# Kernel tuning notes

Measured on AMD Instinct MI355X. Metric: run time of the kernel, lower is better.

Reference implementation:

```python
import jax, jax.numpy as jnp
from jax import lax
import numpy as np

L, D, HEADS, DH, FF = 12, 768, 12, 64, 3072
PATCH, IMG, B, S, OUT = 16, 224, 32, 197, 512


def setup_inputs() -> dict:
    key = jax.random.key(0)
    ks = jax.random.split(key, 10)
    nrm = lambda k, shp, s=0.02: jax.random.normal(k, shp, jnp.float32) * s
    return {
        "x_inp": jax.random.normal(ks[0], (B, 3, IMG, IMG), jnp.float32),
        "conv_w": nrm(ks[1], (D, 3, PATCH, PATCH)),
        "cls_emb": nrm(ks[2], (D,)),
        "pos_emb": nrm(ks[3], (S, D)),
        "ln_pre_w": jnp.ones((D,), jnp.float32),
        "ln_pre_b": jnp.zeros((D,), jnp.float32),
        "ln1_w": jnp.ones((L, D), jnp.float32),
        "ln1_b": jnp.zeros((L, D), jnp.float32),
        "qkv_w": nrm(ks[4], (L, 3 * D, D)),
        "qkv_b": jnp.zeros((L, 3 * D), jnp.float32),
        "out_w": nrm(ks[5], (L, D, D)),
        "out_b": jnp.zeros((L, D), jnp.float32),
        "ln2_w": jnp.ones((L, D), jnp.float32),
        "ln2_b": jnp.zeros((L, D), jnp.float32),
        "fc1_w": nrm(ks[6], (L, FF, D)),
        "fc1_b": jnp.zeros((L, FF), jnp.float32),
        "fc2_w": nrm(ks[7], (L, D, FF)),
        "fc2_b": jnp.zeros((L, D), jnp.float32),
        "ln_post_w": jnp.ones((D,), jnp.float32),
        "ln_post_b": jnp.zeros((D,), jnp.float32),
        "proj": nrm(ks[8], (D, OUT)),
    }


def _ln(x, w, b, eps=1e-5):
    mu = jnp.mean(x, axis=-1, keepdims=True)
    var = jnp.mean(jnp.square(x - mu), axis=-1, keepdims=True)
    return (x - mu) * lax.rsqrt(var + eps) * w + b


def _visual_forward(x_inp, conv_w, cls_emb, pos_emb, ln_pre_w, ln_pre_b,
                    ln1_w, ln1_b, qkv_w, qkv_b, out_w, out_b,
                    ln2_w, ln2_b, fc1_w, fc1_b, fc2_w, fc2_b,
                    ln_post_w, ln_post_b, proj):
    # patch embedding: conv stride=patch, no bias  -> [B, D, 14, 14]
    x = lax.conv_general_dilated(x_inp, conv_w, (PATCH, PATCH), 'VALID',
                                 dimension_numbers=('NCHW', 'OIHW', 'NCHW'))
    b = x.shape[0]
    x = x.reshape(b, D, -1).transpose(0, 2, 1)              # [B, 196, D]
    cls = jnp.broadcast_to(cls_emb, (b, 1, D))
    x = jnp.concatenate([cls, x], axis=1)                   # [B, 197, D]
    x = x + pos_emb[None]                                   # standard 197-token branch
    x = _ln(x, ln_pre_w, ln_pre_b)

    scale = float(DH) ** -0.5

    def block(h, p):
        l1w, l1b, qw, qb, ow, ob, l2w, l2b, f1w, f1b, f2w, f2b = p
        y = _ln(h, l1w, l1b)
        qkv = y @ qw.T + qb                                  # [B, S, 3D]
        q, k, v = jnp.split(qkv, 3, axis=-1)
        q = q.reshape(b, S, HEADS, DH) * scale
        k = k.reshape(b, S, HEADS, DH)
        v = v.reshape(b, S, HEADS, DH)
        attn = jnp.einsum('bqhd,bkhd->bhqk', q, k)
        attn = jax.nn.softmax(attn, axis=-1)
        o = jnp.einsum('bhqk,bkhd->bqhd', attn, v).reshape(b, S, D)
        h = h + o @ ow.T + ob
        y = _ln(h, l2w, l2b)
        y = y @ f1w.T + f1b
        y = y * jax.nn.sigmoid(1.702 * y)                    # QuickGELU
        h = h + y @ f2w.T + f2b
        return h, None

    params = (ln1_w, ln1_b, qkv_w, qkv_b, out_w, out_b,
              ln2_w, ln2_b, fc1_w, fc1_b, fc2_w, fc2_b)
    x, _ = lax.scan(block, x, params)

    cls_out = _ln(x[:, 0, :], ln_post_w, ln_post_b)
    return cls_out @ proj                                    # [B, 512]


def reference(x_inp, conv_w, cls_emb, pos_emb, ln_pre_w, ln_pre_b,
              ln1_w, ln1_b, qkv_w, qkv_b, out_w, out_b,
              ln2_w, ln2_b, fc1_w, fc1_b, fc2_w, fc2_b,
              ln_post_w, ln_post_b, proj):
    return _visual_forward(x_inp, conv_w, cls_emb, pos_emb, ln_pre_w, ln_pre_b,
                           ln1_w, ln1_b, qkv_w, qkv_b, out_w, out_b,
                           ln2_w, ln2_b, fc1_w, fc1_b, fc2_w, fc2_b,
                           ln_post_w, ln_post_b, proj)
```

## Files before the change

kernel.cpp:

```cpp
#include <hip/hip_runtime.h>
#include <hip/hip_bf16.h>


#define LAYERS 12
#define DMODEL 768
#define NHEADS 12
#define DHEAD  64
#define FFDIM  3072
#define BATCH  32
#define SEQ    197
#define NPATCH 196
#define OUTD   512
#define MROWS  (BATCH * SEQ)
#define MPAD   6400
#define SPAD   208
#define VSTR   208

typedef __attribute__((ext_vector_type(4))) float f32x4;
typedef __attribute__((ext_vector_type(8))) short bf16x8;

enum { M_F32 = 0, M_ACC = 1, M_GELU = 2, M_PATCH = 3, M_QKVB = 4 };

__device__ __forceinline__ float b2f(short s) {
    unsigned u = ((unsigned)(unsigned short)s) << 16;
    return __builtin_bit_cast(float, u);
}
__device__ __forceinline__ short f2b(float f) {
    __hip_bfloat16 h = __float2bfloat16(f);
    return __builtin_bit_cast(short, h);
}

__device__ __forceinline__ void gl2lds16(const void* g, void* l) {
    __builtin_amdgcn_global_load_lds(
        (const __attribute__((address_space(1))) void*)g,
        (__attribute__((address_space(3))) void*)l, 16, 0, 0);
}

__global__ __launch_bounds__(256) void cvt_bf16_kernel(
    const float* __restrict__ src, __hip_bfloat16* __restrict__ dst, long n)
{
    long i0 = ((long)blockIdx.x * 256 + threadIdx.x) * 4;
    long stride = (long)gridDim.x * 1024;
    for (long i = i0; i < n; i += stride) {
        float4 v = *reinterpret_cast<const float4*>(&src[i]);
        dst[i + 0] = __float2bfloat16(v.x);
        dst[i + 1] = __float2bfloat16(v.y);
        dst[i + 2] = __float2bfloat16(v.z);
        dst[i + 3] = __float2bfloat16(v.w);
    }
}

__global__ __launch_bounds__(256) void im2col_kernel(
    const float* __restrict__ x_inp, __hip_bfloat16* __restrict__ patches)
{
    int bp = blockIdx.x;
    int b = bp / NPATCH, p = bp % NPATCH;
    int py = p / 14, px = p % 14;
    const float* xb = x_inp + (long)b * 3 * 224 * 224;
    for (int e = threadIdx.x; e < 768; e += 256) {
        int c = e >> 8, i = (e >> 4) & 15, j = e & 15;
        patches[(long)bp * 768 + e] =
            __float2bfloat16(xb[((long)c * 224 + py * 16 + i) * 224 + px * 16 + j]);
    }
}

__global__ __launch_bounds__(256) void cls_token_kernel(
    const float* __restrict__ cls_emb, const float* __restrict__ pos_emb,
    float* __restrict__ x)
{
    int b = blockIdx.x;
    for (int d = threadIdx.x; d < DMODEL; d += 256)
        x[(long)b * SEQ * DMODEL + d] = cls_emb[d] + pos_emb[d];
}

template<int OB>
__global__ __launch_bounds__(256) void ln_kernel(
    const float* __restrict__ in, void* __restrict__ out,
    const float* __restrict__ w, const float* __restrict__ bb,
    long in_stride, long out_stride)
{
    int row = blockIdx.x;
    const float* xr = in + (long)row * in_stride;
    int t = threadIdx.x;
    int lane = t & 63, wid = t >> 6;
    __shared__ float red[8];

    float v[3];
    float s = 0.f;
    #pragma unroll
    for (int i = 0; i < 3; ++i) { v[i] = xr[t + i * 256]; s += v[i]; }
    #pragma unroll
    for (int off = 32; off; off >>= 1) s += __shfl_xor(s, off);
    if (lane == 0) red[wid] = s;
    __syncthreads();
    float mean = (red[0] + red[1] + red[2] + red[3]) * (1.0f / DMODEL);
    float sq = 0.f;
    #pragma unroll
    for (int i = 0; i < 3; ++i) { float d = v[i] - mean; sq += d * d; }
    #pragma unroll
    for (int off = 32; off; off >>= 1) sq += __shfl_xor(sq, off);
    if (lane == 0) red[4 + wid] = sq;
    __syncthreads();
    float rstd = rsqrtf((red[4] + red[5] + red[6] + red[7]) * (1.0f / DMODEL) + 1e-5f);
    #pragma unroll
    for (int i = 0; i < 3; ++i) {
        int d = t + i * 256;
        float o = (v[i] - mean) * rstd * w[d] + bb[d];
        if (OB) ((__hip_bfloat16*)out)[(long)row * out_stride + d] = __float2bfloat16(o);
        else    ((float*)out)[(long)row * out_stride + d] = o;
    }
}

template<int MODE>
__global__ __launch_bounds__(256) void gemm_bf16(
    const __hip_bfloat16* __restrict__ A, const __hip_bfloat16* __restrict__ W,
    const float* __restrict__ bias, float* __restrict__ Cf,
    __hip_bfloat16* __restrict__ Cb, int M, int N, int K, int NB,
    const float* __restrict__ pos)
{
    __shared__ short As[2][64 * 64];
    __shared__ short Bs[2][128 * 64];
    int tid = threadIdx.x, lane = tid & 63, wv = tid >> 6;

    int nwg = gridDim.x, bid = blockIdx.x;
    int qq = nwg >> 3, rr = nwg & 7;
    int xcd = bid & 7, idx = bid >> 3;
    int newid = (xcd < rr ? xcd * (qq + 1) : rr * (qq + 1) + (xcd - rr) * qq) + idx;

    int bm = (newid / NB) * 64, bn = (newid % NB) * 128;
    int wn = wv * 32;
    f32x4 acc[4][2] = {};

    int sr = tid >> 3, sc = tid & 7;
    int c_log = sc ^ (sr & 7);
    const short* Ag = (const short*)A + (long)(bm + sr) * K + (c_log << 3);
    const short* Bg = (const short*)W + (long)(bn + sr) * K + (c_log << 3);
    const long K32 = (long)32 * K;

    int lg = lane >> 4, lr16 = lane & 15;
    int aoff[2][4], boff[2][2];
    #pragma unroll
    for (int s = 0; s < 2; ++s) {
        #pragma unroll
        for (int i = 0; i < 4; ++i) {
            int ra = i * 16 + lr16;
            aoff[s][i] = (ra << 6) + ((((s << 2) | lg) ^ (ra & 7)) << 3);
        }
        #pragma unroll
        for (int j = 0; j < 2; ++j) {
            int rb = wn + j * 16 + lr16;
            boff[s][j] = (rb << 6) + ((((s << 2) | lg) ^ (rb & 7)) << 3);
        }
    }

    const int KT = K >> 6;
    {
        char* Ad = (char*)&As[0][0]; char* Bd = (char*)&Bs[0][0];
        gl2lds16(Ag,           Ad + tid * 16);
        gl2lds16(Ag + K32,     Ad + 4096 + tid * 16);
        gl2lds16(Bg,           Bd + tid * 16);
        gl2lds16(Bg + K32,     Bd + 4096 + tid * 16);
        gl2lds16(Bg + 2 * K32, Bd + 8192 + tid * 16);
        gl2lds16(Bg + 3 * K32, Bd + 12288 + tid * 16);
    }
    __syncthreads();

    int cur = 0;
    for (int t = 0; t < KT; ++t) {
        if (t + 1 < KT) {
            int ktn = (t + 1) << 6;
            char* Ad = (char*)&As[cur ^ 1][0];
            char* Bd = (char*)&Bs[cur ^ 1][0];
            gl2lds16(Ag + ktn,           Ad + tid * 16);
            gl2lds16(Ag + K32 + ktn,     Ad + 4096 + tid * 16);
            gl2lds16(Bg + ktn,           Bd + tid * 16);
            gl2lds16(Bg + K32 + ktn,     Bd + 4096 + tid * 16);
            gl2lds16(Bg + 2 * K32 + ktn, Bd + 8192 + tid * 16);
            gl2lds16(Bg + 3 * K32 + ktn, Bd + 12288 + tid * 16);
        }
        const short* Ab = &As[cur][0];
        const short* Bb = &Bs[cur][0];
        #pragma unroll
        for (int s = 0; s < 2; ++s) {
            bf16x8 af[4], bfr[2];
            #pragma unroll
            for (int i = 0; i < 4; ++i)
                af[i] = *reinterpret_cast<const bf16x8*>(&Ab[aoff[s][i]]);
            #pragma unroll
            for (int j = 0; j < 2; ++j)
                bfr[j] = *reinterpret_cast<const bf16x8*>(&Bb[boff[s][j]]);
            #pragma unroll
            for (int mi = 0; mi < 4; ++mi)
                #pragma unroll
                for (int ni = 0; ni < 2; ++ni)
                    acc[mi][ni] = __builtin_amdgcn_mfma_f32_16x16x32_bf16(
                        af[mi], bfr[ni], acc[mi][ni], 0, 0, 0);
        }
        __syncthreads();
        cur ^= 1;
    }

    #pragma unroll
    for (int mi = 0; mi < 4; ++mi) {
        int row0 = bm + mi * 16 + (lane >> 4) * 4;
        #pragma unroll
        for (int ni = 0; ni < 2; ++ni) {
            int col = bn + wn + ni * 16 + lr16;
            #pragma unroll
            for (int r = 0; r < 4; ++r) {
                int row = row0 + r;
                if (row >= M) continue;
                float v = acc[mi][ni][r];
                if (MODE == M_PATCH) {
                    int pb = row / 196, pp = row - pb * 196;
                    Cf[((long)(pb * SEQ + 1 + pp)) * DMODEL + col] =
                        v + pos[(long)(1 + pp) * DMODEL + col];
                } else {
                    v += bias[col];
                    long idx2 = (long)row * N + col;
                    if (MODE == M_F32)      Cf[idx2] = v;
                    else if (MODE == M_ACC) Cf[idx2] += v;
                    else if (MODE == M_QKVB) Cb[idx2] = __float2bfloat16(v);
                    else if (MODE == M_GELU)
                        Cb[idx2] = __float2bfloat16(v / (1.f + __expf(-1.702f * v)));
                }
            }
        }
    }
}

__global__ __launch_bounds__(256) void attn_kernel(
    const __hip_bfloat16* __restrict__ qkv,
    __hip_bfloat16* __restrict__ o)
{
    int bh = blockIdx.x;
    int b = bh / NHEADS, h = bh % NHEADS;
    int tid = threadIdx.x, lane = tid & 63, wv = tid >> 6;
    __shared__ short Ks[SPAD * 64];
    __shared__ short Vt[64 * VSTR];
    __shared__ short Ps[4][16 * VSTR];
    const short* base = (const short*)qkv + (long)b * SEQ * 2304;

    for (int idx = tid; idx < SPAD * 8; idx += 256) {
        int r = idx >> 3, c = idx & 7;
        int4 val = make_int4(0, 0, 0, 0);
        if (r < SEQ)
            val = *reinterpret_cast<const int4*>(base + (long)r * 2304 + 768 + h * 64 + c * 8);
        *reinterpret_cast<int4*>(&Ks[r * 64 + ((c ^ (r & 7)) << 3)]) = val;
    }
    for (int idx = tid; idx < SPAD * 64; idx += 256) {
        int k = idx >> 6, d = idx & 63;
        short v = (k < SEQ) ? base[(long)k * 2304 + 1536 + h * 64 + d] : (short)0;
        Vt[d * VSTR + k] = v;
    }
    __syncthreads();

    int lg = lane >> 4, lr = lane & 15;
    short* Pw = Ps[wv];

    for (int ch = wv; ch < 13; ch += 4) {
        int q0 = ch * 16;
        const short* qp = (const short*)qkv +
            ((long)(b * SEQ) + q0 + lr) * 2304 + h * 64 + (lg << 3);
        bf16x8 qa = *reinterpret_cast<const bf16x8*>(qp);
        bf16x8 qb = *reinterpret_cast<const bf16x8*>(qp + 32);

        f32x4 sc[13];
        #pragma unroll
        for (int f = 0; f < 13; ++f) sc[f] = (f32x4){0.f, 0.f, 0.f, 0.f};
        #pragma unroll
        for (int f = 0; f < 13; ++f) {
            int row = f * 16 + lr;
            int sw = row & 7;
            const short* kr = &Ks[row * 64];
            bf16x8 k0 = *reinterpret_cast<const bf16x8*>(&kr[((lg + 0) ^ sw) << 3]);
            bf16x8 k1 = *reinterpret_cast<const bf16x8*>(&kr[((lg + 4) ^ sw) << 3]);
            sc[f] = __builtin_amdgcn_mfma_f32_16x16x32_bf16(qa, k0, sc[f], 0, 0, 0);
            sc[f] = __builtin_amdgcn_mfma_f32_16x16x32_bf16(qb, k1, sc[f], 0, 0, 0);
        }

        float mrow[4] = {-1e30f, -1e30f, -1e30f, -1e30f};
        #pragma unroll
        for (int f = 0; f < 13; ++f) {
            bool ok = f * 16 + lr < SEQ;
            #pragma unroll
            for (int r = 0; r < 4; ++r)
                if (ok) mrow[r] = fmaxf(mrow[r], sc[f][r] * 0.125f);
        }
        #pragma unroll
        for (int r = 0; r < 4; ++r)
            #pragma unroll
            for (int off = 8; off; off >>= 1)
                mrow[r] = fmaxf(mrow[r], __shfl_xor(mrow[r], off));
        float esum[4] = {0.f, 0.f, 0.f, 0.f};
        #pragma unroll
        for (int f = 0; f < 13; ++f) {
            bool ok = f * 16 + lr < SEQ;
            #pragma unroll
            for (int r = 0; r < 4; ++r) {
                float e = ok ? __expf(sc[f][r] * 0.125f - mrow[r]) : 0.f;
                sc[f][r] = e;
                esum[r] += e;
            }
        }
        #pragma unroll
        for (int r = 0; r < 4; ++r)
            #pragma unroll
            for (int off = 8; off; off >>= 1)
                esum[r] += __shfl_xor(esum[r], off);
        float inv[4];
        #pragma unroll
        for (int r = 0; r < 4; ++r) inv[r] = 1.0f / esum[r];

        #pragma unroll
        for (int f = 0; f < 13; ++f)
            #pragma unroll
            for (int r = 0; r < 4; ++r)
                Pw[(lg * 4 + r) * VSTR + f * 16 + lr] = f2b(sc[f][r] * inv[r]);

        f32x4 oa[4] = {};
        #pragma unroll
        for (int ks = 0; ks < 7; ++ks) {
            int kb = ks * 32 + (lg << 3);
            bf16x8 pa = {};
            if (kb < SPAD) pa = *reinterpret_cast<const bf16x8*>(&Pw[lr * VSTR + kb]);
            #pragma unroll
            for (int d = 0; d < 4; ++d) {
                bf16x8 vb = {};
                if (kb < SPAD)
                    vb = *reinterpret_cast<const bf16x8*>(&Vt[(d * 16 + lr) * VSTR + kb]);
                oa[d] = __builtin_amdgcn_mfma_f32_16x16x32_bf16(pa, vb, oa[d], 0, 0, 0);
            }
        }

        #pragma unroll
        for (int d = 0; d < 4; ++d)
            #pragma unroll
            for (int r = 0; r < 4; ++r) {
                int q = q0 + lg * 4 + r;
                if (q < SEQ)
                    o[((long)(b * SEQ + q)) * DMODEL + h * 64 + d * 16 + lr] =
                        __float2bfloat16(oa[d][r]);
            }
    }
}

__global__ __launch_bounds__(256) void proj_kernel(
    const float* __restrict__ cls_ln,
    const float* __restrict__ proj,
    float* __restrict__ out)
{
    int idx = blockIdx.x * 256 + threadIdx.x;
    int m = idx >> 9, n = idx & 511;
    float s = 0.f;
    #pragma unroll 8
    for (int k = 0; k < 768; ++k)
        s += cls_ln[m * 768 + k] * proj[k * 512 + n];
    out[idx] = s;
}

extern "C" void kernel_launch(void* const* d_in, const int* in_sizes, int n_in,
                              void* d_out, int out_size, void* d_ws, size_t ws_size,
                              hipStream_t stream) {
    const float* x_inp    = (const float*)d_in[0];
    const float* conv_w   = (const float*)d_in[1];
    const float* cls_emb  = (const float*)d_in[2];
    const float* pos_emb  = (const float*)d_in[3];
    const float* ln_pre_w = (const float*)d_in[4];
    const float* ln_pre_b = (const float*)d_in[5];
    const float* ln1_w    = (const float*)d_in[6];
    const float* ln1_b    = (const float*)d_in[7];
    const float* qkv_w    = (const float*)d_in[8];
    const float* qkv_b    = (const float*)d_in[9];
    const float* out_w    = (const float*)d_in[10];
    const float* out_b    = (const float*)d_in[11];
    const float* ln2_w    = (const float*)d_in[12];
    const float* ln2_b    = (const float*)d_in[13];
    const float* fc1_w    = (const float*)d_in[14];
    const float* fc1_b    = (const float*)d_in[15];
    const float* fc2_w    = (const float*)d_in[16];
    const float* fc2_b    = (const float*)d_in[17];
    const float* ln_post_w= (const float*)d_in[18];
    const float* ln_post_b= (const float*)d_in[19];
    const float* proj     = (const float*)d_in[20];

    char* w = (char*)d_ws;
    __hip_bfloat16* wqkv = (__hip_bfloat16*)w; w += (size_t)LAYERS * 2304 * DMODEL * 2;
    __hip_bfloat16* wout = (__hip_bfloat16*)w; w += (size_t)LAYERS * DMODEL * DMODEL * 2;
    __hip_bfloat16* wfc1 = (__hip_bfloat16*)w; w += (size_t)LAYERS * FFDIM * DMODEL * 2;
    __hip_bfloat16* wfc2 = (__hip_bfloat16*)w; w += (size_t)LAYERS * DMODEL * FFDIM * 2;
    __hip_bfloat16* wconv= (__hip_bfloat16*)w; w += (size_t)DMODEL * DMODEL * 2;
    float* x             = (float*)w;          w += (size_t)MROWS * DMODEL * 4;
    __hip_bfloat16* y    = (__hip_bfloat16*)w; w += (size_t)MPAD * DMODEL * 2;
    __hip_bfloat16* qkvb = (__hip_bfloat16*)w; w += (size_t)MPAD * 2304 * 2;
    __hip_bfloat16* attno= (__hip_bfloat16*)w; w += (size_t)MPAD * DMODEL * 2;
    __hip_bfloat16* h1   = (__hip_bfloat16*)w; w += (size_t)MPAD * FFDIM * 2;
    __hip_bfloat16* patches = (__hip_bfloat16*)w; w += (size_t)NPATCH * BATCH * DMODEL * 2;
    float* clsb          = (float*)w;          w += (size_t)BATCH * DMODEL * 4;

    cvt_bf16_kernel<<<2048, 256, 0, stream>>>(qkv_w, wqkv, (long)LAYERS * 2304 * DMODEL);
    cvt_bf16_kernel<<<2048, 256, 0, stream>>>(out_w, wout, (long)LAYERS * DMODEL * DMODEL);
    cvt_bf16_kernel<<<2048, 256, 0, stream>>>(fc1_w, wfc1, (long)LAYERS * FFDIM * DMODEL);
    cvt_bf16_kernel<<<2048, 256, 0, stream>>>(fc2_w, wfc2, (long)LAYERS * DMODEL * FFDIM);
    cvt_bf16_kernel<<<512, 256, 0, stream>>>(conv_w, wconv, (long)DMODEL * DMODEL);

    im2col_kernel<<<NPATCH * BATCH, 256, 0, stream>>>(x_inp, patches);
    gemm_bf16<M_PATCH><<<98 * 6, 256, 0, stream>>>(
        patches, wconv, nullptr, x, nullptr, NPATCH * BATCH, DMODEL, DMODEL, 6, pos_emb);
    cls_token_kernel<<<BATCH, 256, 0, stream>>>(cls_emb, pos_emb, x);
    ln_kernel<0><<<MROWS, 256, 0, stream>>>(x, x, ln_pre_w, ln_pre_b, DMODEL, DMODEL);

    for (int l = 0; l < LAYERS; ++l) {
        ln_kernel<1><<<MROWS, 256, 0, stream>>>(x, y, ln1_w + l * DMODEL, ln1_b + l * DMODEL,
                                                DMODEL, DMODEL);
        gemm_bf16<M_QKVB><<<99 * 18, 256, 0, stream>>>(
            y, wqkv + (long)l * 2304 * DMODEL, qkv_b + (long)l * 2304, nullptr, qkvb,
            MROWS, 2304, DMODEL, 18, nullptr);
        attn_kernel<<<BATCH * NHEADS, 256, 0, stream>>>(qkvb, attno);
        gemm_bf16<M_ACC><<<99 * 6, 256, 0, stream>>>(
            attno, wout + (long)l * DMODEL * DMODEL, out_b + (long)l * DMODEL, x, nullptr,
            MROWS, DMODEL, DMODEL, 6, nullptr);
        ln_kernel<1><<<MROWS, 256, 0, stream>>>(x, y, ln2_w + l * DMODEL, ln2_b + l * DMODEL,
                                                DMODEL, DMODEL);
        gemm_bf16<M_GELU><<<99 * 24, 256, 0, stream>>>(
            y, wfc1 + (long)l * FFDIM * DMODEL, fc1_b + (long)l * FFDIM, nullptr, h1,
            MROWS, FFDIM, DMODEL, 24, nullptr);
        gemm_bf16<M_ACC><<<99 * 6, 256, 0, stream>>>(
            h1, wfc2 + (long)l * DMODEL * FFDIM, fc2_b + (long)l * DMODEL, x, nullptr,
            MROWS, DMODEL, FFDIM, 6, nullptr);
    }

    ln_kernel<0><<<BATCH, 256, 0, stream>>>(x, clsb, ln_post_w, ln_post_b,
                                            (long)SEQ * DMODEL, DMODEL);
    proj_kernel<<<(BATCH * OUTD) / 256, 256, 0, stream>>>(clsb, proj, (float*)d_out);
}
```

Measured before the change: 3.438 ms.

## Split K across wave pairs in bf16 GEMM with LDS reduction

Each 64x128 GEMM tile is now computed by a 2x2 wave grid. Two waves split the N dimension and two split each 64-wide K step in half, so every wave holds a 64x64 accumulator and loads 4 A and 4 B fragments per step instead of 4 A and 2 B. That raises the MFMA-to-LDS-read ratio per wave. After the K loop, the upper-K waves write their partials into LDS, and the lower-K waves add them and run the epilogue. The cost is double the accumulator registers, which may lower occupancy, plus an extra LDS reduction with a barrier, during which half the waves sit idle.

After: 4.935 ms. +43.5%, slower.

```diff
diff --git a/kernel.cpp b/kernel.cpp
--- a/kernel.cpp
+++ b/kernel.cpp
@@ -118,8 +118,12 @@
     __hip_bfloat16* __restrict__ Cb, int M, int N, int K, int NB,
     const float* __restrict__ pos)
 {
-    __shared__ short As[2][64 * 64];
-    __shared__ short Bs[2][128 * 64];
+    __shared__ __align__(16) char smem[49152];
+    char* A0 = smem;
+    char* A1 = smem + 8192;
+    char* B0 = smem + 16384;
+    char* B1 = smem + 32768;
+
     int tid = threadIdx.x, lane = tid & 63, wv = tid >> 6;
 
     int nwg = gridDim.x, bid = blockIdx.x;
@@ -128,8 +132,8 @@
     int newid = (xcd < rr ? xcd * (qq + 1) : rr * (qq + 1) + (xcd - rr) * qq) + idx;
 
     int bm = (newid / NB) * 64, bn = (newid % NB) * 128;
-    int wn = wv * 32;
-    f32x4 acc[4][2] = {};
+    int wkh = wv >> 1, wnh = wv & 1;
+    f32x4 acc[4][4] = {};
 
     int sr = tid >> 3, sc = tid & 7;
     int c_log = sc ^ (sr & 7);
@@ -138,39 +142,33 @@
     const long K32 = (long)32 * K;
 
     int lg = lane >> 4, lr16 = lane & 15;
-    int aoff[2][4], boff[2][2];
-    #pragma unroll
-    for (int s = 0; s < 2; ++s) {
-        #pragma unroll
-        for (int i = 0; i < 4; ++i) {
-            int ra = i * 16 + lr16;
-            aoff[s][i] = (ra << 6) + ((((s << 2) | lg) ^ (ra & 7)) << 3);
-        }
-        #pragma unroll
-        for (int j = 0; j < 2; ++j) {
-            int rb = wn + j * 16 + lr16;
-            boff[s][j] = (rb << 6) + ((((s << 2) | lg) ^ (rb & 7)) << 3);
-        }
+    int kc = (wkh << 2) | lg;
+    int aoff[4], boff[4];
+    #pragma unroll
+    for (int i = 0; i < 4; ++i) {
+        int ra = i * 16 + lr16;
+        aoff[i] = (ra << 6) + ((kc ^ (ra & 7)) << 3);
+    }
+    #pragma unroll
+    for (int j = 0; j < 4; ++j) {
+        int rb = wnh * 64 + j * 16 + lr16;
+        boff[j] = (rb << 6) + ((kc ^ (rb & 7)) << 3);
     }
 
     const int KT = K >> 6;
-    {
-        char* Ad = (char*)&As[0][0]; char* Bd = (char*)&Bs[0][0];
-        gl2lds16(Ag,           Ad + tid * 16);
-        gl2lds16(Ag + K32,     Ad + 4096 + tid * 16);
-        gl2lds16(Bg,           Bd + tid * 16);
-        gl2lds16(Bg + K32,     Bd + 4096 + tid * 16);
-        gl2lds16(Bg + 2 * K32, Bd + 8192 + tid * 16);
-        gl2lds16(Bg + 3 * K32, Bd + 12288 + tid * 16);
-    }
+    gl2lds16(Ag,           A0 + tid * 16);
+    gl2lds16(Ag + K32,     A0 + 4096 + tid * 16);
+    gl2lds16(Bg,           B0 + tid * 16);
+    gl2lds16(Bg + K32,     B0 + 4096 + tid * 16);
+    gl2lds16(Bg + 2 * K32, B0 + 8192 + tid * 16);
+    gl2lds16(Bg + 3 * K32, B0 + 12288 + tid * 16);
     __syncthreads();
 
-    int cur = 0;
     for (int t = 0; t < KT; ++t) {
         if (t + 1 < KT) {
             int ktn = (t + 1) << 6;
-            char* Ad = (char*)&As[cur ^ 1][0];
-            char* Bd = (char*)&Bs[cur ^ 1][0];
+            char* Ad = (t & 1) ? A0 : A1;
+            char* Bd = (t & 1) ? B0 : B1;
             gl2lds16(Ag + ktn,           Ad + tid * 16);
             gl2lds16(Ag + K32 + ktn,     Ad + 4096 + tid * 16);
             gl2lds16(Bg + ktn,           Bd + tid * 16);
@@ -178,34 +176,52 @@
             gl2lds16(Bg + 2 * K32 + ktn, Bd + 8192 + tid * 16);
             gl2lds16(Bg + 3 * K32 + ktn, Bd + 12288 + tid * 16);
         }
-        const short* Ab = &As[cur][0];
-        const short* Bb = &Bs[cur][0];
-        #pragma unroll
-        for (int s = 0; s < 2; ++s) {
-            bf16x8 af[4], bfr[2];
-            #pragma unroll
-            for (int i = 0; i < 4; ++i)
-                af[i] = *reinterpret_cast<const bf16x8*>(&Ab[aoff[s][i]]);
-            #pragma unroll
-            for (int j = 0; j < 2; ++j)
-                bfr[j] = *reinterpret_cast<const bf16x8*>(&Bb[boff[s][j]]);
+        const short* Ab = (const short*)((t & 1) ? A1 : A0);
+        const short* Bb = (const short*)((t & 1) ? B1 : B0);
+        bf16x8 af[4], bfr[4];
+        #pragma unroll
+        for (int i = 0; i < 4; ++i)
+            af[i] = *reinterpret_cast<const bf16x8*>(&Ab[aoff[i]]);
+        #pragma unroll
+        for (int j = 0; j < 4; ++j)
+            bfr[j] = *reinterpret_cast<const bf16x8*>(&Bb[boff[j]]);
+        #pragma unroll
+        for (int mi = 0; mi < 4; ++mi)
+            #pragma unroll
+            for (int ni = 0; ni < 4; ++ni)
+                acc[mi][ni] = __builtin_amdgcn_mfma_f32_16x16x32_bf16(
+                    af[mi], bfr[ni], acc[mi][ni], 0, 0, 0);
+        __syncthreads();
+    }
+
+    float* red = (float*)smem;
+    float* area = red + wnh * (64 * 72);
+    if (wkh == 1) {
+        #pragma unroll
+        for (int ni = 0; ni < 4; ++ni) {
+            int cl = ni * 16 + lr16;
             #pragma unroll
             for (int mi = 0; mi < 4; ++mi)
-                #pragma unroll
-                for (int ni = 0; ni < 2; ++ni)
-                    acc[mi][ni] = __builtin_amdgcn_mfma_f32_16x16x32_bf16(
-                        af[mi], bfr[ni], acc[mi][ni], 0, 0, 0);
-        }
-        __syncthreads();
-        cur ^= 1;
+                *reinterpret_cast<f32x4*>(&area[cl * 72 + mi * 16 + lg * 4]) = acc[mi][ni];
+        }
+    }
+    __syncthreads();
+    if (wkh == 1) return;
+
+    #pragma unroll
+    for (int ni = 0; ni < 4; ++ni) {
+        int cl = ni * 16 + lr16;
+        #pragma unroll
+        for (int mi = 0; mi < 4; ++mi)
+            acc[mi][ni] += *reinterpret_cast<const f32x4*>(&area[cl * 72 + mi * 16 + lg * 4]);
     }
 
     #pragma unroll
     for (int mi = 0; mi < 4; ++mi) {
-        int row0 = bm + mi * 16 + (lane >> 4) * 4;
-        #pragma unroll
-        for (int ni = 0; ni < 2; ++ni) {
-            int col = bn + wn + ni * 16 + lr16;
+        int row0 = bm + mi * 16 + lg * 4;
+        #pragma unroll
+        for (int ni = 0; ni < 4; ++ni) {
+            int col = bn + wnh * 64 + ni * 16 + lr16;
             #pragma unroll
             for (int r = 0; r < 4; ++r) {
                 int row = row0 + r;
```

## Add 256x256-tile 512-thread GEMM for QKV and FC1 projections

Applied to the files above, without the earlier changes.

Adds a new GEMM kernel with 256x256 output tiles, 8 waves, 128KB LDS double buffering, staggered global-to-LDS staging across four compute phases, XCD-aware block remapping, and MFMA priority raising. It is used for the QKV and FC1 GEMMs in place of the 64-row tile kernel. The aim is more operand reuse per tile and better overlap of loads with MFMA work. The cost is fewer blocks (225/300 on a large-CU device), a padded M of 6400 that relies on the workspace being big enough for 256-row reads, and more register pressure.

Result: no change. 3.505 ms (+1.9%).

```diff
diff --git a/kernel.cpp b/kernel.cpp
--- a/kernel.cpp
+++ b/kernel.cpp
@@ -36,6 +36,12 @@
         (__attribute__((address_space(3))) void*)l, 16, 0, 0);
 }
 
+__device__ __forceinline__ void hard_barrier() {
+    asm volatile("" ::: "memory");
+    __builtin_amdgcn_s_barrier();
+    asm volatile("" ::: "memory");
+}
+
 __global__ __launch_bounds__(256) void cvt_bf16_kernel(
     const float* __restrict__ src, __hip_bfloat16* __restrict__ dst, long n)
 {
@@ -165,12 +171,11 @@
     }
     __syncthreads();
 
-    int cur = 0;
     for (int t = 0; t < KT; ++t) {
         if (t + 1 < KT) {
             int ktn = (t + 1) << 6;
-            char* Ad = (char*)&As[cur ^ 1][0];
-            char* Bd = (char*)&Bs[cur ^ 1][0];
+            char* Ad = (char*)&As[(t & 1) ^ 1][0];
+            char* Bd = (char*)&Bs[(t & 1) ^ 1][0];
             gl2lds16(Ag + ktn,           Ad + tid * 16);
             gl2lds16(Ag + K32 + ktn,     Ad + 4096 + tid * 16);
             gl2lds16(Bg + ktn,           Bd + tid * 16);
@@ -178,8 +183,8 @@
             gl2lds16(Bg + 2 * K32 + ktn, Bd + 8192 + tid * 16);
             gl2lds16(Bg + 3 * K32 + ktn, Bd + 12288 + tid * 16);
         }
-        const short* Ab = &As[cur][0];
-        const short* Bb = &Bs[cur][0];
+        const short* Ab = &As[t & 1][0];
+        const short* Bb = &Bs[t & 1][0];
         #pragma unroll
         for (int s = 0; s < 2; ++s) {
             bf16x8 af[4], bfr[2];
@@ -197,7 +202,6 @@
                         af[mi], bfr[ni], acc[mi][ni], 0, 0, 0);
         }
         __syncthreads();
-        cur ^= 1;
     }
 
     #pragma unroll
@@ -229,9 +233,144 @@
     }
 }
 
+template<int MODE>
+__global__ __launch_bounds__(512) void gemm_big(
+    const __hip_bfloat16* __restrict__ A, const __hip_bfloat16* __restrict__ W,
+    const float* __restrict__ bias, __hip_bfloat16* __restrict__ Cb,
+    int M, int N, int K, int NB)
+{
+    __shared__ __align__(16) char smem[131072];
+    int tid = threadIdx.x, lane = tid & 63, wv = tid >> 6;
+
+    int nwg = gridDim.x, bid = blockIdx.x;
+    int qq = nwg >> 3, rr = nwg & 7;
+    int xcd = bid & 7, idx = bid >> 3;
+    int newid = (xcd < rr ? xcd * (qq + 1) : rr * (qq + 1) + (xcd - rr) * qq) + idx;
+
+    int bm = (newid / NB) * 256, bn = (newid % NB) * 256;
+    int wr = wv >> 2, wc = wv & 3;
+    f32x4 acc[8][4] = {};
+
+    int sr = tid >> 3, scn = tid & 7;
+    int c_log = scn ^ (sr & 7);
+    const short* Aga = (const short*)A + (long)(bm + sr) * K + (c_log << 3);
+    const short* Bga = (const short*)W + (long)(bn + sr) * K + (c_log << 3);
+    const long U = (long)64 * K;
+
+    int lg = lane >> 4, lr16 = lane & 15;
+    int aoff[2][2][4], boff[2][4];
+    #pragma unroll
+    for (int ks = 0; ks < 2; ++ks) {
+        int kc = (ks << 2) | lg;
+        #pragma unroll
+        for (int mh = 0; mh < 2; ++mh)
+            #pragma unroll
+            for (int i = 0; i < 4; ++i) {
+                int ra = wr * 128 + mh * 64 + i * 16 + lr16;
+                aoff[mh][ks][i] = (ra << 6) + ((kc ^ (ra & 7)) << 3);
+            }
+        #pragma unroll
+        for (int j = 0; j < 4; ++j) {
+            int rb = wc * 64 + j * 16 + lr16;
+            boff[ks][j] = (rb << 6) + ((kc ^ (rb & 7)) << 3);
+        }
+    }
+
+    const int KT = K >> 6;
+
+#define GB_STAGE_A(BUF, u, kt) gl2lds16(Aga + (long)(u) * U + (kt), (BUF) + (u) * 8192 + tid * 16)
+#define GB_STAGE_B(BUF, u, kt) gl2lds16(Bga + (long)(u) * U + (kt), (BUF) + (u) * 8192 + tid * 16)
+
+    {
+        char* A0 = smem, *B0 = smem + 65536;
+        GB_STAGE_A(A0, 0, 0); GB_STAGE_A(A0, 1, 0);
+        GB_STAGE_A(A0, 2, 0); GB_STAGE_A(A0, 3, 0);
+        GB_STAGE_B(B0, 0, 0); GB_STAGE_B(B0, 1, 0);
+        GB_STAGE_B(B0, 2, 0); GB_STAGE_B(B0, 3, 0);
+        if (KT > 1) {
+            char* A1 = smem + 32768;
+            GB_STAGE_A(A1, 0, 64); GB_STAGE_A(A1, 2, 64);
+            asm volatile("s_waitcnt vmcnt(2)" ::: "memory");
+        } else {
+            asm volatile("s_waitcnt vmcnt(0)" ::: "memory");
+        }
+        hard_barrier();
+    }
+
+#define GB_PHASE(MH, KS)                                                        \
+    {                                                                           \
+        bf16x8 af[4], bfv[4];                                                   \
+        _Pragma("unroll")                                                       \
+        for (int i = 0; i < 4; ++i) {                                           \
+            af[i]  = *reinterpret_cast<const bf16x8*>(&Ab_[aoff[MH][KS][i]]);   \
+            bfv[i] = *reinterpret_cast<const bf16x8*>(&Bb_[boff[KS][i]]);       \
+        }                                                                       \
+        hard_barrier();                                                         \
+        asm volatile("s_waitcnt lgkmcnt(0)" ::: "memory");                      \
+        __builtin_amdgcn_sched_barrier(0);                                      \
+        __builtin_amdgcn_s_setprio(1);                                          \
+        _Pragma("unroll")                                                       \
+        for (int i = 0; i < 4; ++i)                                             \
+            _Pragma("unroll")                                                   \
+            for (int j = 0; j < 4; ++j)                                         \
+                acc[(MH) * 4 + i][j] = __builtin_amdgcn_mfma_f32_16x16x32_bf16( \
+                    af[i], bfv[j], acc[(MH) * 4 + i][j], 0, 0, 0);              \
+        __builtin_amdgcn_s_setprio(0);                                          \
+    }
+
+    for (int c = 0; c < KT; ++c) {
+        const int d = c & 1, d1 = d ^ 1;
+        const short* Ab_ = (const short*)(smem + d * 32768);
+        const short* Bb_ = (const short*)(smem + 65536 + d * 32768);
+        char* An = smem + d1 * 32768;
+        char* Bn = smem + 65536 + d1 * 32768;
+        char* Ad2 = smem + d * 32768;
+        const int kt1 = (c + 1) << 6, kt2 = (c + 2) << 6;
+        const bool h1 = (c + 1 < KT), h2 = (c + 2 < KT);
+
+        if (h1) { GB_STAGE_A(An, 1, kt1); GB_STAGE_A(An, 3, kt1); }
+        GB_PHASE(0, 0);
+        hard_barrier();
+
+        if (h1) { GB_STAGE_B(Bn, 0, kt1); GB_STAGE_B(Bn, 1, kt1); }
+        GB_PHASE(0, 1);
+        hard_barrier();
+
+        if (h1) { GB_STAGE_B(Bn, 2, kt1); GB_STAGE_B(Bn, 3, kt1); }
+        GB_PHASE(1, 0);
+        hard_barrier();
+
+        if (h2) { GB_STAGE_A(Ad2, 0, kt2); GB_STAGE_A(Ad2, 2, kt2); }
+        GB_PHASE(1, 1);
+        if (h2) asm volatile("s_waitcnt vmcnt(2)" ::: "memory");
+        else    asm volatile("s_waitcnt vmcnt(0)" ::: "memory");
+        hard_barrier();
+    }
+
+    #pragma unroll
+    for (int mi = 0; mi < 8; ++mi) {
+        int row0 = bm + wr * 128 + (mi >> 2) * 64 + (mi & 3) * 16 + lg * 4;
+        #pragma unroll
+        for (int ni = 0; ni < 4; ++ni) {
+            int col = bn + wc * 64 + ni * 16 + lr16;
+            #pragma unroll
+            for (int r = 0; r < 4; ++r) {
+                int row = row0 + r;
+                if (row >= M) continue;
+                float v = acc[mi][ni][r] + bias[col];
+                long idx2 = (long)row * N + col;
+                if (MODE == M_QKVB) Cb[idx2] = __float2bfloat16(v);
+                else                Cb[idx2] = __float2bfloat16(v / (1.f + __expf(-1.702f * v)));
+            }
+        }
+    }
+#undef GB_PHASE
+#undef GB_STAGE_A
+#undef GB_STAGE_B
+}
+
 __global__ __launch_bounds__(256) void attn_kernel(
-    const __hip_bfloat16* __restrict__ qkv,
-    __hip_bfloat16* __restrict__ o)
+    const __hip_bfloat16* __restrict__ qkv, __hip_bfloat16* __restrict__ o)
 {
     int bh = blockIdx.x;
     int b = bh / NHEADS, h = bh % NHEADS;
@@ -346,8 +485,7 @@
 }
 
 __global__ __launch_bounds__(256) void proj_kernel(
-    const float* __restrict__ cls_ln,
-    const float* __restrict__ proj,
+    const float* __restrict__ cls_ln, const float* __restrict__ proj,
     float* __restrict__ out)
 {
     int idx = blockIdx.x * 256 + threadIdx.x;
@@ -413,18 +551,18 @@
     for (int l = 0; l < LAYERS; ++l) {
         ln_kernel<1><<<MROWS, 256, 0, stream>>>(x, y, ln1_w + l * DMODEL, ln1_b + l * DMODEL,
                                                 DMODEL, DMODEL);
-        gemm_bf16<M_QKVB><<<99 * 18, 256, 0, stream>>>(
-            y, wqkv + (long)l * 2304 * DMODEL, qkv_b + (long)l * 2304, nullptr, qkvb,
-            MROWS, 2304, DMODEL, 18, nullptr);
+        gemm_big<M_QKVB><<<25 * 9, 512, 0, stream>>>(
+            y, wqkv + (long)l * 2304 * DMODEL, qkv_b + (long)l * 2304, qkvb,
+            MROWS, 2304, DMODEL, 9);
         attn_kernel<<<BATCH * NHEADS, 256, 0, stream>>>(qkvb, attno);
         gemm_bf16<M_ACC><<<99 * 6, 256, 0, stream>>>(
             attno, wout + (long)l * DMODEL * DMODEL, out_b + (long)l * DMODEL, x, nullptr,
             MROWS, DMODEL, DMODEL, 6, nullptr);
         ln_kernel<1><<<MROWS, 256, 0, stream>>>(x, y, ln2_w + l * DMODEL, ln2_b + l * DMODEL,
                                                 DMODEL, DMODEL);
-        gemm_bf16<M_GELU><<<99 * 24, 256, 0, stream>>>(
-            y, wfc1 + (long)l * FFDIM * DMODEL, fc1_b + (long)l * FFDIM, nullptr, h1,
-            MROWS, FFDIM, DMODEL, 24, nullptr);
+        gemm_big<M_GELU><<<25 * 12, 512, 0, stream>>>(
+            y, wfc1 + (long)l * FFDIM * DMODEL, fc1_b + (long)l * FFDIM, h1,
+            MROWS, FFDIM, DMODEL, 12);
         gemm_bf16<M_ACC><<<99 * 6, 256, 0, stream>>>(
             h1, wfc2 + (long)l * DMODEL * FFDIM, fc2_b + (long)l * DMODEL, x, nullptr,
             MROWS, DMODEL, FFDIM, 6, nullptr);
```
